# Performance work log

Measured on AMD Instinct MI355X. Metric: run time of the kernel, lower is better.

## Reference

```python
import jax, jax.numpy as jnp
import numpy as np

VOCAB = 128
HID = 1024
STD = 0.01


def setup_inputs() -> dict:
    key = jax.random.key(0)
    ks = jax.random.split(key, 9)
    X = jax.random.randint(ks[0], (64, 512), 0, VOCAB, dtype=jnp.int32)
    def w(k, shape):
        return jax.random.normal(k, shape, dtype=jnp.float32) * STD
    return {
        "X": X,
        # reset gate
        "Wr_x": w(ks[1], (VOCAB, HID)), "Wr_h": w(ks[2], (HID, HID)), "b_r": jnp.zeros(HID, jnp.float32),
        # update gate
        "Wz_x": w(ks[3], (VOCAB, HID)), "Wz_h": w(ks[4], (HID, HID)), "b_z": jnp.zeros(HID, jnp.float32),
        # candidate
        "Wh_x": w(ks[5], (VOCAB, HID)), "Wh_h": w(ks[6], (HID, HID)), "b_h": jnp.zeros(HID, jnp.float32),
        # output head
        "W_o": w(ks[7], (HID, VOCAB)), "b_o": jnp.zeros(VOCAB, jnp.float32),
    }


def reference(X, Wr_x, Wr_h, b_r, Wz_x, Wz_h, b_z, Wh_x, Wh_h, b_h, W_o, b_o):
    B, T = X.shape
    # one-hot encode all timesteps: (T, B, V)
    Xoh = jax.nn.one_hot(X.T, VOCAB, dtype=jnp.float32)

    def step(h, x_t):
        # x_t: (B, V), h: (B, H)
        r = jax.nn.sigmoid(x_t @ Wr_x + h @ Wr_h + b_r)
        z = jax.nn.sigmoid(x_t @ Wz_x + h @ Wz_h + b_z)
        h_tilde = jnp.tanh(x_t @ Wh_x + (r * h) @ Wh_h + b_h)
        h_new = z * h + (1.0 - z) * h_tilde
        out = h_new @ W_o + b_o  # (B, V)
        return h_new, out

    h0 = jnp.zeros((B, HID), jnp.float32)
    _, outs = jax.lax.scan(step, h0, Xoh)  # outs: (T, B, V)
    return jnp.transpose(outs, (1, 0, 2))  # (B, T, V)
```

## Files before the change

kernel.cpp:

```cpp
#include <hip/hip_runtime.h>

#define HID   1024
#define TLEN  512
#define VOC   128
#define NBLK  256
#define NW    32
#define LDSK  1032
#define HBUF  (64 * HID)

typedef __bf16 bf16_t;
typedef __attribute__((ext_vector_type(8))) __bf16 bf16x8;
typedef __attribute__((ext_vector_type(4))) float  f32x4;

__device__ __forceinline__ float sigmoid_fast(float x) {
  return 1.0f / (1.0f + __expf(-x));
}
__device__ __forceinline__ float tanh_fast(float x) {
  float e = __expf(-2.0f * x);
  return (1.0f - e) / (1.0f + e);
}

union PairU { bf16_t b[2]; unsigned u; };

__device__ __forceinline__ void l1_inv() {
  asm volatile("buffer_inv" ::: "memory");
}

__device__ __forceinline__ bf16x8 ldw(const bf16_t* p) {
  return *reinterpret_cast<const bf16x8*>(p);
}

__device__ __forceinline__ void wait_flags(const unsigned* f, unsigned tgt) {
  const volatile unsigned* p =
      (const volatile unsigned*)(f + (threadIdx.x & 31));
  for (;;) {
    l1_inv();
    unsigned v = *p;
    if (__all((int)(v - tgt) >= 0)) break;
  }
}

__device__ __forceinline__ void publish(unsigned* fw, unsigned v) {
  __syncthreads();
  if (threadIdx.x == 0) *(volatile unsigned*)fw = v;
}

#define MFMA(a, b, c) __builtin_amdgcn_mfma_f32_16x16x32_bf16((a), (b), (c), 0, 0, 0)

__global__ void __launch_bounds__(256, 1)
gru_team(const int* __restrict__ X,
         const float* __restrict__ Wr_x, const float* __restrict__ Wr_h, const float* __restrict__ b_r,
         const float* __restrict__ Wz_x, const float* __restrict__ Wz_h, const float* __restrict__ b_z,
         const float* __restrict__ Wh_x, const float* __restrict__ Wh_h, const float* __restrict__ b_h,
         const float* __restrict__ W_o,  const float* __restrict__ b_o,
         float* __restrict__ out,
         bf16_t* __restrict__ hring, bf16_t* __restrict__ rh_bf,
         bf16_t* __restrict__ wz_bf, bf16_t* __restrict__ wo_bf,
         unsigned* __restrict__ flags)
{
  __shared__ __align__(16) bf16_t Wbuf[2 * 32 * LDSK];
  __shared__ __align__(16) float  Obuf[8][16][16];
  __shared__ int s_role;

  unsigned* fH     = flags;
  unsigned* fR     = flags + 32;
  unsigned* cnt    = flags + 128;
  unsigned* winner = flags + 160;
  unsigned* ready  = flags + 168;
  unsigned* done   = flags + 172;

  const int tid  = threadIdx.x;
  const int lane = tid & 63;
  const int wv   = tid >> 6;
  const int n16  = lane & 15;
  const int q    = lane >> 4;
  const int aoff = (wv * 16 + n16) * HID + q * 8;

  int bi[4];
#pragma unroll
  for (int i = 0; i < 4; ++i) bi[i] = wv * 16 + q * 4 + i;

  if (tid == 0) {
    unsigned xcc;
    asm volatile("s_getreg_b32 %0, hwreg(HW_REG_XCC_ID)" : "=s"(xcc));
    xcc &= 7u;
    unsigned idx = __hip_atomic_fetch_add(&cnt[xcc], 1u, __ATOMIC_RELAXED, __HIP_MEMORY_SCOPE_AGENT);
    if (idx == NW - 1) {
      unsigned exp = 0u;
      __hip_atomic_compare_exchange_strong(winner, &exp, xcc + 1u,
          __ATOMIC_RELAXED, __ATOMIC_RELAXED, __HIP_MEMORY_SCOPE_AGENT);
    }
    unsigned w;
    do {
      w = __hip_atomic_load(winner, __ATOMIC_RELAXED, __HIP_MEMORY_SCOPE_AGENT);
      __builtin_amdgcn_s_sleep(1);
    } while (w == 0u);
    s_role = (xcc == w - 1u && idx < NW) ? (int)idx : -1;
  }
  __syncthreads();
  const int role = s_role;

  if (role < 0) {
    __shared__ volatile int sdone;
    if (tid == 0) sdone = 0;
    __syncthreads();
    float a0 = 1.0f + (float)tid, a1 = 1.1f, a2 = 1.2f, a3 = 1.3f;
    const float m = 1.0000001f, c = 1e-7f;
    while (!sdone) {
      for (int it = 0; it < 1024; ++it) {
        a0 = __builtin_fmaf(a0, m, c);
        a1 = __builtin_fmaf(a1, m, c);
        a2 = __builtin_fmaf(a2, m, c);
        a3 = __builtin_fmaf(a3, m, c);
      }
      if (tid == 0 &&
          __hip_atomic_load(done, __ATOMIC_RELAXED, __HIP_MEMORY_SCOPE_AGENT) != 0u)
        sdone = 1;
    }
    asm volatile("" :: "v"(a0), "v"(a1), "v"(a2), "v"(a3));
    return;
  }

  const int s  = role;
  const int c0 = s * 32;

  if (tid == 0) {
    *(volatile unsigned*)&fH[s] = 0u;
    *(volatile unsigned*)&fR[s] = 0u;
  }

  for (int idx = tid; idx < 32 * HID; idx += 256) {
    int n = idx & 31, k = idx >> 5;
    int r = (n & 1) * 16 + (n >> 1);
    Wbuf[r * LDSK + k]             = (bf16_t)Wr_h[k * HID + c0 + n];
    Wbuf[32 * LDSK + r * LDSK + k] = (bf16_t)Wh_h[k * HID + c0 + n];
  }
  bf16_t* wzs = wz_bf + s * (32 * 1024);
  for (int idx = tid; idx < 32 * HID; idx += 256) {
    int n = idx & 31, k = idx >> 5;
    int r = (n & 1) * 16 + (n >> 1);
    wzs[r * 1024 + k] = (bf16_t)Wz_h[k * HID + c0 + n];
  }
  if (s < 8) {
    bf16_t* wos = wo_bf + s * (16 * 1024);
    for (int idx = tid; idx < 16 * HID; idx += 256) {
      int n = idx & 15, k = idx >> 4;
      wos[n * 1024 + k] = (bf16_t)W_o[k * VOC + s * 16 + n];
    }
  }
  const int j0 = c0 + 2 * n16;
#pragma unroll
  for (int i = 0; i < 4; ++i) {
    PairU zz; zz.b[0] = (bf16_t)0.f; zz.b[1] = (bf16_t)0.f;
    *reinterpret_cast<PairU*>(hring + bi[i] * HID + j0) = zz;
  }
  __syncthreads();

  if (tid == 0) {
    __hip_atomic_fetch_add(ready, 1u, __ATOMIC_RELAXED, __HIP_MEMORY_SCOPE_AGENT);
    while (__hip_atomic_load(ready, __ATOMIC_RELAXED, __HIP_MEMORY_SCOPE_AGENT) < NW)
      __builtin_amdgcn_s_sleep(1);
  }
  __syncthreads();
  if (tid == 0) *(volatile unsigned*)&fH[s] = 1u;

  const float br0 = b_r[j0], br1 = b_r[j0 + 1];
  const float bz0 = b_z[j0], bz1 = b_z[j0 + 1];
  const float bh0 = b_h[j0], bh1 = b_h[j0 + 1];
  const bf16_t* wr0 = &Wbuf[n16 * LDSK + q * 8];
  const bf16_t* wr1 = &Wbuf[(16 + n16) * LDSK + q * 8];
  const bf16_t* wh0 = &Wbuf[32 * LDSK + n16 * LDSK + q * 8];
  const bf16_t* wh1 = &Wbuf[32 * LDSK + (16 + n16) * LDSK + q * 8];
  const bf16_t* wz0 = wzs + n16 * 1024 + q * 8;
  const bf16_t* wz1 = wzs + (16 + n16) * 1024 + q * 8;
  const bf16_t* rhrow = rh_bf + aoff;

  const int rt = s >> 3, vt = s & 7;
  const bool outw = (wv == rt);
  const bf16_t* wop = wo_bf + vt * (16 * 1024) + n16 * 1024 + q * 8;
  const float bo = b_o[vt * 16 + n16];

  f32x4 hm0 = {0.f,0.f,0.f,0.f}, hm1 = {0.f,0.f,0.f,0.f};

  for (int t = 0; t < TLEN; ++t) {
    float gr0[4], gr1[4], gz0[4], gz1[4], gh0[4], gh1[4];
#pragma unroll
    for (int i = 0; i < 4; ++i) {
      int xb = X[bi[i] * TLEN + t];
      gr0[i] = Wr_x[xb * HID + j0]; gr1[i] = Wr_x[xb * HID + j0 + 1];
      gz0[i] = Wz_x[xb * HID + j0]; gz1[i] = Wz_x[xb * HID + j0 + 1];
      gh0[i] = Wh_x[xb * HID + j0]; gh1[i] = Wh_x[xb * HID + j0 + 1];
    }

    wait_flags(fH, (unsigned)(t + 1));
    const bf16_t* hrow = hring + (t & 1) * HBUF + aoff;
    bf16x8 areg[32];
#pragma unroll
    for (int kk = 0; kk < 32; ++kk) areg[kk] = ldw(hrow + kk * 32);

    f32x4 aR0 = {0.f,0.f,0.f,0.f}, aR1 = {0.f,0.f,0.f,0.f};
    f32x4 bR0 = {0.f,0.f,0.f,0.f}, bR1 = {0.f,0.f,0.f,0.f};
#pragma unroll
    for (int kk = 0; kk < 16; ++kk) {
      aR0 = MFMA(areg[kk],      ldw(wr0 + kk * 32),        aR0);
      aR1 = MFMA(areg[kk],      ldw(wr1 + kk * 32),        aR1);
      bR0 = MFMA(areg[kk + 16], ldw(wr0 + (kk + 16) * 32), bR0);
      bR1 = MFMA(areg[kk + 16], ldw(wr1 + (kk + 16) * 32), bR1);
    }
    aR0 += bR0; aR1 += bR1;
#pragma unroll
    for (int i = 0; i < 4; ++i) {
      float r0 = sigmoid_fast(aR0[i] + br0 + gr0[i]);
      float r1 = sigmoid_fast(aR1[i] + br1 + gr1[i]);
      PairU c;
      c.b[0] = (bf16_t)(r0 * hm0[i]);
      c.b[1] = (bf16_t)(r1 * hm1[i]);
      *reinterpret_cast<PairU*>(rh_bf + bi[i] * HID + j0) = c;
    }
    publish(&fR[s], (unsigned)(t + 1));

    if (outw && t) {
      f32x4 oa = {0.f,0.f,0.f,0.f}, ob2 = {0.f,0.f,0.f,0.f};
#pragma unroll
      for (int kk = 0; kk < 16; ++kk) {
        oa  = MFMA(areg[kk],      ldw(wop + kk * 32),        oa);
        ob2 = MFMA(areg[kk + 16], ldw(wop + (kk + 16) * 32), ob2);
      }
      oa += ob2;
      const int oi = (t - 1) & 7;
#pragma unroll
      for (int i = 0; i < 4; ++i) Obuf[oi][q * 4 + i][n16] = oa[i] + bo;
      if (oi == 7) {
        const int rb = t - 8;
#pragma unroll
        for (int k = 0; k < 8; ++k)
#pragma unroll
          for (int i = 0; i < 4; ++i)
            out[(bi[i] * TLEN + rb + k) * VOC + vt * 16 + n16] =
                Obuf[k][q * 4 + i][n16];
      }
    }

    f32x4 aZ0 = {0.f,0.f,0.f,0.f}, aZ1 = {0.f,0.f,0.f,0.f};
    f32x4 bZ0 = {0.f,0.f,0.f,0.f}, bZ1 = {0.f,0.f,0.f,0.f};
#pragma unroll
    for (int kk = 0; kk < 16; ++kk) {
      aZ0 = MFMA(areg[kk],      ldw(wz0 + kk * 32),        aZ0);
      aZ1 = MFMA(areg[kk],      ldw(wz1 + kk * 32),        aZ1);
      bZ0 = MFMA(areg[kk + 16], ldw(wz0 + (kk + 16) * 32), bZ0);
      bZ1 = MFMA(areg[kk + 16], ldw(wz1 + (kk + 16) * 32), bZ1);
    }
    aZ0 += bZ0; aZ1 += bZ1;
    f32x4 z0, z1;
#pragma unroll
    for (int i = 0; i < 4; ++i) {
      z0[i] = sigmoid_fast(aZ0[i] + bz0 + gz0[i]);
      z1[i] = sigmoid_fast(aZ1[i] + bz1 + gz1[i]);
    }

    wait_flags(fR, (unsigned)(t + 1));
    bf16x8 breg[32];
#pragma unroll
    for (int kk = 0; kk < 32; ++kk) breg[kk] = ldw(rhrow + kk * 32);
    f32x4 aH0 = {0.f,0.f,0.f,0.f}, aH1 = {0.f,0.f,0.f,0.f};
    f32x4 bH0 = {0.f,0.f,0.f,0.f}, bH1 = {0.f,0.f,0.f,0.f};
#pragma unroll
    for (int kk = 0; kk < 16; ++kk) {
      aH0 = MFMA(breg[kk],      ldw(wh0 + kk * 32),        aH0);
      aH1 = MFMA(breg[kk],      ldw(wh1 + kk * 32),        aH1);
      bH0 = MFMA(breg[kk + 16], ldw(wh0 + (kk + 16) * 32), bH0);
      bH1 = MFMA(breg[kk + 16], ldw(wh1 + (kk + 16) * 32), bH1);
    }
    aH0 += bH0; aH1 += bH1;
    bf16_t* hnext = hring + ((t + 1) & 1) * HBUF;
#pragma unroll
    for (int i = 0; i < 4; ++i) {
      float ht0 = tanh_fast(aH0[i] + bh0 + gh0[i]);
      float ht1 = tanh_fast(aH1[i] + bh1 + gh1[i]);
      float hn0 = z0[i] * hm0[i] + (1.f - z0[i]) * ht0;
      float hn1 = z1[i] * hm1[i] + (1.f - z1[i]) * ht1;
      hm0[i] = hn0; hm1[i] = hn1;
      PairU c; c.b[0] = (bf16_t)hn0; c.b[1] = (bf16_t)hn1;
      *reinterpret_cast<PairU*>(hnext + bi[i] * HID + j0) = c;
    }
    publish(&fH[s], (unsigned)(t + 2));
  }

  if (outw) {
    wait_flags(fH, (unsigned)(TLEN + 1));
    const bf16_t* hrow = hring + (TLEN & 1) * HBUF + aoff;
    bf16x8 areg[32];
#pragma unroll
    for (int kk = 0; kk < 32; ++kk) areg[kk] = ldw(hrow + kk * 32);
    f32x4 oa = {0.f,0.f,0.f,0.f}, ob2 = {0.f,0.f,0.f,0.f};
#pragma unroll
    for (int kk = 0; kk < 16; ++kk) {
      oa  = MFMA(areg[kk],      ldw(wop + kk * 32),        oa);
      ob2 = MFMA(areg[kk + 16], ldw(wop + (kk + 16) * 32), ob2);
    }
    oa += ob2;
#pragma unroll
    for (int i = 0; i < 4; ++i) Obuf[7][q * 4 + i][n16] = oa[i] + bo;
#pragma unroll
    for (int k = 0; k < 8; ++k)
#pragma unroll
      for (int i = 0; i < 4; ++i)
        out[(bi[i] * TLEN + 504 + k) * VOC + vt * 16 + n16] =
            Obuf[k][q * 4 + i][n16];
  }

  if (s == 0 && tid == 0)
    __hip_atomic_store(done, 1u, __ATOMIC_RELAXED, __HIP_MEMORY_SCOPE_AGENT);

  __builtin_amdgcn_fence(__ATOMIC_RELEASE, "agent");
}

extern "C" void kernel_launch(void* const* d_in, const int* in_sizes, int n_in,
                              void* d_out, int out_size, void* d_ws, size_t ws_size,
                              hipStream_t stream) {
  const int*   X    = (const int*)d_in[0];
  const float* Wr_x = (const float*)d_in[1];
  const float* Wr_h = (const float*)d_in[2];
  const float* b_r  = (const float*)d_in[3];
  const float* Wz_x = (const float*)d_in[4];
  const float* Wz_h = (const float*)d_in[5];
  const float* b_z  = (const float*)d_in[6];
  const float* Wh_x = (const float*)d_in[7];
  const float* Wh_h = (const float*)d_in[8];
  const float* b_h  = (const float*)d_in[9];
  const float* W_o  = (const float*)d_in[10];
  const float* b_o  = (const float*)d_in[11];

  char* ws = (char*)d_ws;
  unsigned* flags = (unsigned*)ws;
  bf16_t*   hring = (bf16_t*)(ws + 4096);
  bf16_t*   rh_bf = (bf16_t*)(ws + 4096 + 2 * HBUF * sizeof(bf16_t));
  bf16_t*   wz_bf = (bf16_t*)(ws + 4096 + 3 * HBUF * sizeof(bf16_t));
  bf16_t*   wo_bf = (bf16_t*)(ws + 4096 + 3 * HBUF * sizeof(bf16_t)
                              + (size_t)NW * 32 * HID * sizeof(bf16_t));

  hipMemsetAsync(ws, 0, 4096, stream);

  gru_team<<<NBLK, 256, 0, stream>>>(
      X, Wr_x, Wr_h, b_r, Wz_x, Wz_h, b_z, Wh_x, Wh_h, b_h, W_o, b_o,
      (float*)d_out, hring, rh_bf, wz_bf, wo_bf, flags);
}
```

Measured before the change: 9.453 ms.

## Split batch across four XCD teams of single-wave blocks

The kernel drops the single 32-block team on one XCD, where each 256-thread block handled all 64 batch rows. It now forms up to four independent teams on separate XCDs, each handling 16 batch rows with 64-thread blocks and its own h/rh ring buffers and flags. The spinning filler blocks on idle CUs are removed. The aim is to spread the recurrent work across XCDs so each team's per-step MFMA and load work is smaller, at the cost of running more cross-block flag syncs in parallel, with the Wz_h and W_o bf16 copies shared through global memory written only by team 0.

```diff
diff --git a/kernel.cpp b/kernel.cpp
--- a/kernel.cpp
+++ b/kernel.cpp
@@ -4,9 +4,11 @@
 #define TLEN  512
 #define VOC   128
 #define NBLK  256
-#define NW    32
+#define NT    4
+#define NB    32
+#define MR    16
 #define LDSK  1032
-#define HBUF  (64 * HID)
+#define HBUF  (MR * HID)
 
 typedef __bf16 bf16_t;
 typedef __attribute__((ext_vector_type(8))) __bf16 bf16x8;
@@ -47,118 +49,105 @@
 
 #define MFMA(a, b, c) __builtin_amdgcn_mfma_f32_16x16x32_bf16((a), (b), (c), 0, 0, 0)
 
-__global__ void __launch_bounds__(256, 1)
-gru_team(const int* __restrict__ X,
-         const float* __restrict__ Wr_x, const float* __restrict__ Wr_h, const float* __restrict__ b_r,
-         const float* __restrict__ Wz_x, const float* __restrict__ Wz_h, const float* __restrict__ b_z,
-         const float* __restrict__ Wh_x, const float* __restrict__ Wh_h, const float* __restrict__ b_h,
-         const float* __restrict__ W_o,  const float* __restrict__ b_o,
-         float* __restrict__ out,
-         bf16_t* __restrict__ hring, bf16_t* __restrict__ rh_bf,
-         bf16_t* __restrict__ wz_bf, bf16_t* __restrict__ wo_bf,
-         unsigned* __restrict__ flags)
+__global__ void __launch_bounds__(64, 1)
+gru_mt(const int* __restrict__ X,
+       const float* __restrict__ Wr_x, const float* __restrict__ Wr_h, const float* __restrict__ b_r,
+       const float* __restrict__ Wz_x, const float* __restrict__ Wz_h, const float* __restrict__ b_z,
+       const float* __restrict__ Wh_x, const float* __restrict__ Wh_h, const float* __restrict__ b_h,
+       const float* __restrict__ W_o,  const float* __restrict__ b_o,
+       float* __restrict__ out,
+       bf16_t* __restrict__ hring, bf16_t* __restrict__ rh_bf,
+       bf16_t* __restrict__ wz_bf, bf16_t* __restrict__ wo_bf,
+       unsigned* __restrict__ flags)
 {
   __shared__ __align__(16) bf16_t Wbuf[2 * 32 * LDSK];
   __shared__ __align__(16) float  Obuf[8][16][16];
-  __shared__ int s_role;
-
-  unsigned* fH     = flags;
-  unsigned* fR     = flags + 32;
-  unsigned* cnt    = flags + 128;
-  unsigned* winner = flags + 160;
-  unsigned* ready  = flags + 168;
-  unsigned* done   = flags + 172;
+  __shared__ int s_team, s_slot;
+
+  unsigned* cnt   = flags + 1024;
+  unsigned* tcnt  = flags + 1536;
+  unsigned* xteam = flags + 2048;
+  unsigned* ready = flags + 3072;
 
   const int tid  = threadIdx.x;
-  const int lane = tid & 63;
-  const int wv   = tid >> 6;
-  const int n16  = lane & 15;
-  const int q    = lane >> 4;
-  const int aoff = (wv * 16 + n16) * HID + q * 8;
+  const int n16  = tid & 15;
+  const int q    = tid >> 4;
 
   int bi[4];
 #pragma unroll
-  for (int i = 0; i < 4; ++i) bi[i] = wv * 16 + q * 4 + i;
+  for (int i = 0; i < 4; ++i) bi[i] = q * 4 + i;
 
   if (tid == 0) {
     unsigned xcc;
     asm volatile("s_getreg_b32 %0, hwreg(HW_REG_XCC_ID)" : "=s"(xcc));
     xcc &= 7u;
-    unsigned idx = __hip_atomic_fetch_add(&cnt[xcc], 1u, __ATOMIC_RELAXED, __HIP_MEMORY_SCOPE_AGENT);
-    if (idx == NW - 1) {
-      unsigned exp = 0u;
-      __hip_atomic_compare_exchange_strong(winner, &exp, xcc + 1u,
-          __ATOMIC_RELAXED, __ATOMIC_RELAXED, __HIP_MEMORY_SCOPE_AGENT);
-    }
-    unsigned w;
+    unsigned idx = __hip_atomic_fetch_add(&cnt[xcc * 32], 1u,
+        __ATOMIC_RELAXED, __HIP_MEMORY_SCOPE_AGENT);
+    if (idx == NB - 1) {
+      unsigned tcl = __hip_atomic_fetch_add(tcnt, 1u,
+          __ATOMIC_RELAXED, __HIP_MEMORY_SCOPE_AGENT);
+      __hip_atomic_store(&xteam[xcc * 32], (tcl < NT) ? (tcl + 1u) : 0xFFu,
+          __ATOMIC_RELAXED, __HIP_MEMORY_SCOPE_AGENT);
+    }
+    unsigned v;
     do {
-      w = __hip_atomic_load(winner, __ATOMIC_RELAXED, __HIP_MEMORY_SCOPE_AGENT);
+      v = __hip_atomic_load(&xteam[xcc * 32], __ATOMIC_RELAXED,
+                            __HIP_MEMORY_SCOPE_AGENT);
       __builtin_amdgcn_s_sleep(1);
-    } while (w == 0u);
-    s_role = (xcc == w - 1u && idx < NW) ? (int)idx : -1;
+    } while (v == 0u);
+    s_team = (v == 0xFFu) ? -1 : (int)(v - 1u);
+    s_slot = (int)idx;
   }
   __syncthreads();
-  const int role = s_role;
-
-  if (role < 0) {
-    __shared__ volatile int sdone;
-    if (tid == 0) sdone = 0;
-    __syncthreads();
-    float a0 = 1.0f + (float)tid, a1 = 1.1f, a2 = 1.2f, a3 = 1.3f;
-    const float m = 1.0000001f, c = 1e-7f;
-    while (!sdone) {
-      for (int it = 0; it < 1024; ++it) {
-        a0 = __builtin_fmaf(a0, m, c);
-        a1 = __builtin_fmaf(a1, m, c);
-        a2 = __builtin_fmaf(a2, m, c);
-        a3 = __builtin_fmaf(a3, m, c);
-      }
-      if (tid == 0 &&
-          __hip_atomic_load(done, __ATOMIC_RELAXED, __HIP_MEMORY_SCOPE_AGENT) != 0u)
-        sdone = 1;
-    }
-    asm volatile("" :: "v"(a0), "v"(a1), "v"(a2), "v"(a3));
-    return;
-  }
-
-  const int s  = role;
+  const int tau = s_team;
+  if (tau < 0) return;
+  const int s  = s_slot;
   const int c0 = s * 32;
+
+  unsigned* fH = flags + tau * 256;
+  unsigned* fR = fH + 64;
 
   if (tid == 0) {
     *(volatile unsigned*)&fH[s] = 0u;
     *(volatile unsigned*)&fR[s] = 0u;
   }
 
-  for (int idx = tid; idx < 32 * HID; idx += 256) {
+  for (int idx = tid; idx < 32 * HID; idx += 64) {
     int n = idx & 31, k = idx >> 5;
     int r = (n & 1) * 16 + (n >> 1);
     Wbuf[r * LDSK + k]             = (bf16_t)Wr_h[k * HID + c0 + n];
     Wbuf[32 * LDSK + r * LDSK + k] = (bf16_t)Wh_h[k * HID + c0 + n];
   }
-  bf16_t* wzs = wz_bf + s * (32 * 1024);
-  for (int idx = tid; idx < 32 * HID; idx += 256) {
-    int n = idx & 31, k = idx >> 5;
-    int r = (n & 1) * 16 + (n >> 1);
-    wzs[r * 1024 + k] = (bf16_t)Wz_h[k * HID + c0 + n];
-  }
-  if (s < 8) {
-    bf16_t* wos = wo_bf + s * (16 * 1024);
-    for (int idx = tid; idx < 16 * HID; idx += 256) {
-      int n = idx & 15, k = idx >> 4;
-      wos[n * 1024 + k] = (bf16_t)W_o[k * VOC + s * 16 + n];
-    }
-  }
+  bf16_t* wzs = wz_bf + s * (32 * HID);
+  if (tau == 0) {
+    for (int idx = tid; idx < 32 * HID; idx += 64) {
+      int n = idx & 31, k = idx >> 5;
+      int r = (n & 1) * 16 + (n >> 1);
+      wzs[r * HID + k] = (bf16_t)Wz_h[k * HID + c0 + n];
+    }
+    if (s < 8) {
+      bf16_t* wos = wo_bf + s * (16 * HID);
+      for (int idx = tid; idx < 16 * HID; idx += 64) {
+        int n = idx & 15, k = idx >> 4;
+        wos[n * HID + k] = (bf16_t)W_o[k * VOC + s * 16 + n];
+      }
+    }
+  }
+
+  bf16_t* hT  = hring + tau * (2 * HBUF);
+  bf16_t* rhT = rh_bf + tau * HBUF;
   const int j0 = c0 + 2 * n16;
 #pragma unroll
   for (int i = 0; i < 4; ++i) {
     PairU zz; zz.b[0] = (bf16_t)0.f; zz.b[1] = (bf16_t)0.f;
-    *reinterpret_cast<PairU*>(hring + bi[i] * HID + j0) = zz;
+    *reinterpret_cast<PairU*>(hT + bi[i] * HID + j0) = zz;
   }
   __syncthreads();
 
   if (tid == 0) {
     __hip_atomic_fetch_add(ready, 1u, __ATOMIC_RELAXED, __HIP_MEMORY_SCOPE_AGENT);
-    while (__hip_atomic_load(ready, __ATOMIC_RELAXED, __HIP_MEMORY_SCOPE_AGENT) < NW)
+    while (__hip_atomic_load(ready, __ATOMIC_RELAXED, __HIP_MEMORY_SCOPE_AGENT)
+           < (unsigned)(NT * NB))
       __builtin_amdgcn_s_sleep(1);
   }
   __syncthreads();
@@ -171,14 +160,16 @@
   const bf16_t* wr1 = &Wbuf[(16 + n16) * LDSK + q * 8];
   const bf16_t* wh0 = &Wbuf[32 * LDSK + n16 * LDSK + q * 8];
   const bf16_t* wh1 = &Wbuf[32 * LDSK + (16 + n16) * LDSK + q * 8];
-  const bf16_t* wz0 = wzs + n16 * 1024 + q * 8;
-  const bf16_t* wz1 = wzs + (16 + n16) * 1024 + q * 8;
-  const bf16_t* rhrow = rh_bf + aoff;
-
-  const int rt = s >> 3, vt = s & 7;
-  const bool outw = (wv == rt);
-  const bf16_t* wop = wo_bf + vt * (16 * 1024) + n16 * 1024 + q * 8;
-  const float bo = b_o[vt * 16 + n16];
+  const bf16_t* wz0 = wzs + n16 * HID + q * 8;
+  const bf16_t* wz1 = wzs + (16 + n16) * HID + q * 8;
+  const int  aoff  = n16 * HID + q * 8;
+  const bf16_t* rhrow = rhT + aoff;
+
+  const bool outw = (s < 8);
+  const int  vt   = s;
+  const bf16_t* wop = wo_bf + vt * (16 * HID) + n16 * HID + q * 8;
+  const float bo = outw ? b_o[vt * 16 + n16] : 0.f;
+  const int  gb0 = tau * MR;
 
   f32x4 hm0 = {0.f,0.f,0.f,0.f}, hm1 = {0.f,0.f,0.f,0.f};
 
@@ -186,14 +177,14 @@
     float gr0[4], gr1[4], gz0[4], gz1[4], gh0[4], gh1[4];
 #pragma unroll
     for (int i = 0; i < 4; ++i) {
-      int xb = X[bi[i] * TLEN + t];
+      int xb = X[(gb0 + bi[i]) * TLEN + t];
       gr0[i] = Wr_x[xb * HID + j0]; gr1[i] = Wr_x[xb * HID + j0 + 1];
       gz0[i] = Wz_x[xb * HID + j0]; gz1[i] = Wz_x[xb * HID + j0 + 1];
       gh0[i] = Wh_x[xb * HID + j0]; gh1[i] = Wh_x[xb * HID + j0 + 1];
     }
 
     wait_flags(fH, (unsigned)(t + 1));
-    const bf16_t* hrow = hring + (t & 1) * HBUF + aoff;
+    const bf16_t* hrow = hT + (t & 1) * HBUF + aoff;
     bf16x8 areg[32];
 #pragma unroll
     for (int kk = 0; kk < 32; ++kk) areg[kk] = ldw(hrow + kk * 32);
@@ -215,7 +206,7 @@
       PairU c;
       c.b[0] = (bf16_t)(r0 * hm0[i]);
       c.b[1] = (bf16_t)(r1 * hm1[i]);
-      *reinterpret_cast<PairU*>(rh_bf + bi[i] * HID + j0) = c;
+      *reinterpret_cast<PairU*>(rhT + bi[i] * HID + j0) = c;
     }
     publish(&fR[s], (unsigned)(t + 1));
 
@@ -229,15 +220,16 @@
       oa += ob2;
       const int oi = (t - 1) & 7;
 #pragma unroll
-      for (int i = 0; i < 4; ++i) Obuf[oi][q * 4 + i][n16] = oa[i] + bo;
+      for (int i = 0; i < 4; ++i) Obuf[oi][bi[i]][n16] = oa[i] + bo;
       if (oi == 7) {
         const int rb = t - 8;
 #pragma unroll
-        for (int k = 0; k < 8; ++k)
-#pragma unroll
-          for (int i = 0; i < 4; ++i)
-            out[(bi[i] * TLEN + rb + k) * VOC + vt * 16 + n16] =
-                Obuf[k][q * 4 + i][n16];
+        for (int m = 0; m < 32; ++m) {
+          int e = m * 64 + tid;
+          int row = e >> 7, tt = (e >> 4) & 7, cc = e & 15;
+          out[((gb0 + row) * TLEN + rb + tt) * VOC + vt * 16 + cc] =
+              Obuf[tt][row][cc];
+        }
       }
     }
 
@@ -272,7 +264,7 @@
       bH1 = MFMA(breg[kk + 16], ldw(wh1 + (kk + 16) * 32), bH1);
     }
     aH0 += bH0; aH1 += bH1;
-    bf16_t* hnext = hring + ((t + 1) & 1) * HBUF;
+    bf16_t* hnext = hT + ((t + 1) & 1) * HBUF;
 #pragma unroll
     for (int i = 0; i < 4; ++i) {
       float ht0 = tanh_fast(aH0[i] + bh0 + gh0[i]);
@@ -288,7 +280,7 @@
 
   if (outw) {
     wait_flags(fH, (unsigned)(TLEN + 1));
-    const bf16_t* hrow = hring + (TLEN & 1) * HBUF + aoff;
+    const bf16_t* hrow = hT + (TLEN & 1) * HBUF + aoff;
     bf16x8 areg[32];
 #pragma unroll
     for (int kk = 0; kk < 32; ++kk) areg[kk] = ldw(hrow + kk * 32);
@@ -300,17 +292,15 @@
     }
     oa += ob2;
 #pragma unroll
-    for (int i = 0; i < 4; ++i) Obuf[7][q * 4 + i][n16] = oa[i] + bo;
-#pragma unroll
-    for (int k = 0; k < 8; ++k)
-#pragma unroll
-      for (int i = 0; i < 4; ++i)
-        out[(bi[i] * TLEN + 504 + k) * VOC + vt * 16 + n16] =
-            Obuf[k][q * 4 + i][n16];
-  }
-
-  if (s == 0 && tid == 0)
-    __hip_atomic_store(done, 1u, __ATOMIC_RELAXED, __HIP_MEMORY_SCOPE_AGENT);
+    for (int i = 0; i < 4; ++i) Obuf[7][bi[i]][n16] = oa[i] + bo;
+#pragma unroll
+    for (int m = 0; m < 32; ++m) {
+      int e = m * 64 + tid;
+      int row = e >> 7, tt = (e >> 4) & 7, cc = e & 15;
+      out[((gb0 + row) * TLEN + 504 + tt) * VOC + vt * 16 + cc] =
+          Obuf[tt][row][cc];
+    }
+  }
 
   __builtin_amdgcn_fence(__ATOMIC_RELEASE, "agent");
 }
@@ -333,15 +323,15 @@
 
   char* ws = (char*)d_ws;
   unsigned* flags = (unsigned*)ws;
-  bf16_t*   hring = (bf16_t*)(ws + 4096);
-  bf16_t*   rh_bf = (bf16_t*)(ws + 4096 + 2 * HBUF * sizeof(bf16_t));
-  bf16_t*   wz_bf = (bf16_t*)(ws + 4096 + 3 * HBUF * sizeof(bf16_t));
-  bf16_t*   wo_bf = (bf16_t*)(ws + 4096 + 3 * HBUF * sizeof(bf16_t)
-                              + (size_t)NW * 32 * HID * sizeof(bf16_t));
-
-  hipMemsetAsync(ws, 0, 4096, stream);
-
-  gru_team<<<NBLK, 256, 0, stream>>>(
+  bf16_t*   hring = (bf16_t*)(ws + 16384);
+  bf16_t*   rh_bf = (bf16_t*)(ws + 16384 + (size_t)NT * 2 * HBUF * sizeof(bf16_t));
+  bf16_t*   wz_bf = (bf16_t*)(ws + 16384 + (size_t)NT * 3 * HBUF * sizeof(bf16_t));
+  bf16_t*   wo_bf = (bf16_t*)(ws + 16384 + (size_t)NT * 3 * HBUF * sizeof(bf16_t)
+                              + (size_t)NB * 32 * HID * sizeof(bf16_t));
+
+  hipMemsetAsync(ws, 0, 16384, stream);
+
+  gru_mt<<<NBLK, 64, 0, stream>>>(
       X, Wr_x, Wr_h, b_r, Wz_x, Wz_h, b_z, Wh_x, Wh_h, b_h, W_o, b_o,
       (float*)d_out, hring, rh_bf, wz_bf, wo_bf, flags);
 }
```

Result: faster. 7.889 ms (-16.5%).
